# Optimization experiments

Measured on AMD Instinct MI355X. Metric: run time of the kernel, lower is better.

## Reference

```python
import jax, jax.numpy as jnp
import numpy as np

EPS = 1e-6


def setup_inputs() -> dict:
    key = jax.random.key(0)
    kH, kE1, kE2, kM, kW = jax.random.split(key, 5)
    B, N, D, E, L = 16, 2048, 64, 32768, 2
    H = jax.random.normal(kH, (B, N, D), dtype=jnp.float32)
    src = jax.random.randint(kE1, (B, 1, E), 0, N)
    dst = jax.random.randint(kE2, (B, 1, E), 0, N)
    edge_index = jnp.concatenate([src, dst], axis=1)  # [B, 2, E]
    m = jax.random.uniform(kM, (B, E), dtype=jnp.float32)
    W = jax.random.normal(kW, (L, D, D), dtype=jnp.float32) * (1.0 / np.sqrt(D))
    return {"H": H, "edge_index": edge_index, "m": m, "W": W}


def reference(H, edge_index, m, W):
    # H: [B, N, D]; edge_index: [B, 2, E] int; m: [B, E]; W: [L, D, D]
    B, N, _ = H.shape
    L = W.shape[0]
    bidx = jnp.arange(B)[:, None]          # [B, 1] broadcasts against [B, E]
    src = edge_index[:, 0, :]
    dst = edge_index[:, 1, :]
    A = jnp.zeros((B, N, N), dtype=H.dtype)
    # batched scatter: A[b, src, dst] = m; A[b, dst, src] = m (symmetric fill)
    A = A.at[bidx, src, dst].set(m)
    A = A.at[bidx, dst, src].set(m)
    A = A + jnp.eye(N, dtype=H.dtype)[None]  # add self loops
    deg = jnp.clip(A.sum(axis=-1), EPS)       # [B, N]
    dis = deg ** -0.5
    A_norm = dis[:, :, None] * A * dis[:, None, :]  # D^-1/2 A D^-1/2
    X = H
    for l in range(L):
        X = jnp.einsum('bnm,bmd->bnd', A_norm, X)
        X = jnp.einsum('bnd,ed->bne', X, W[l])  # Linear: X @ W^T
        if l < L - 1:
            X = jax.nn.gelu(X, approximate=False)  # torch GELU (exact erf); dropout in eval mode
    return X
```

## Files before the change

### kernel.cpp

```cpp
#include <hip/hip_runtime.h>
#include <stdint.h>
#include <math.h>

#define BATCH 16
#define NNODE 2048
#define DDIM  64
#define NEDGE 32768
#define SEG   32
#define SLOTS 128
#define NROWS (BATCH*NNODE)
#define RPB   128

__global__ void k_build(const int* __restrict__ ei, const float* __restrict__ m,
                        uint32_t* __restrict__ cnt4, uint2* __restrict__ entries) {
    __shared__ uint32_t cntS[RPB];
    __shared__ uint32_t keyS[RPB][SEG];
    __shared__ float    valS[RPB][SEG];

    int b  = blockIdx.x & 15;
    int gh = blockIdx.x >> 4;
    int r0 = (gh >> 2) * RPB;
    int q  = gh & 3;
    int t  = threadIdx.x;

    if (t < RPB) cntS[t] = 0u;
    __syncthreads();

    const int*   eb = ei + (size_t)b * 2 * NEDGE;
    const float* mb = m  + (size_t)b * NEDGE;
    int e0 = q * (NEDGE / 4);

    for (int i = 0; i < 4; ++i) {
        int e4 = e0 + i * 2048 + t * 4;
        int4   s4 = *(const int4*)(eb + e4);
        int4   d4 = *(const int4*)(eb + NEDGE + e4);
        float4 m4 = *(const float4*)(mb + e4);
        #pragma unroll
        for (int j = 0; j < 4; ++j) {
            int   src = j == 0 ? s4.x : j == 1 ? s4.y : j == 2 ? s4.z : s4.w;
            int   dst = j == 0 ? d4.x : j == 1 ? d4.y : j == 2 ? d4.z : d4.w;
            float mv  = j == 0 ? m4.x : j == 1 ? m4.y : j == 2 ? m4.z : m4.w;
            int e  = e4 + j;
            int rs = src - r0;
            if ((unsigned)rs < RPB) {
                uint32_t p = atomicAdd(&cntS[rs], 1u);
                if (p < SEG) { keyS[rs][p] = (uint32_t)dst | ((uint32_t)e << 11); valS[rs][p] = mv; }
            }
            int rd = dst - r0;
            if ((unsigned)rd < RPB) {
                uint32_t p = atomicAdd(&cntS[rd], 1u);
                if (p < SEG) { keyS[rd][p] = (uint32_t)src | ((uint32_t)(NEDGE + e) << 11); valS[rd][p] = mv; }
            }
        }
    }
    __syncthreads();

    int lane = t & 63;
    int wid  = t >> 6;
    int pos  = lane & 31;
    int sub  = lane >> 5;
    for (int rr = 0; rr < 8; ++rr) {
        int r  = wid * 16 + rr * 2 + sub;
        int rg = b * NNODE + r0 + r;
        int k  = (int)min(cntS[r], (uint32_t)SEG);
        size_t base = (size_t)rg * SLOTS + q * SEG;
        if (pos < k)
            entries[base + pos] = make_uint2(keyS[r][pos], __float_as_uint(valS[r][pos]));
        if (pos == 0) cnt4[rg * 4 + q] = (uint32_t)k;
    }
}

__global__ void k_dedupe(const uint32_t* __restrict__ cnt4, uint2* __restrict__ entries,
                         uint32_t* __restrict__ cnt_fin,
                         float* __restrict__ dis, float* __restrict__ self) {
    int b    = blockIdx.x & 15;
    int w    = b * NNODE + (blockIdx.x >> 4) * 4 + (threadIdx.x >> 6);
    int lane = threadIdx.x & 63;
    uint4 kq = ((const uint4*)cnt4)[w];
    int k0 = (int)kq.x, k1 = (int)kq.y, k2 = (int)kq.z, k3 = (int)kq.w;
    size_t base = (size_t)w * SLOTS;
    int pos = lane & 31;
    int klo = (lane < 32) ? k0 : k1;
    int khi = (lane < 32) ? k2 : k3;

    uint32_t key0 = 0u, key1 = 0u;
    float v0 = 0.f, v1 = 0.f;
    bool a0 = pos < klo;
    bool a1 = pos < khi;
    if (a0) { uint2 kv = entries[base + lane];      key0 = kv.x; v0 = __uint_as_float(kv.y); }
    if (a1) { uint2 kv = entries[base + 64 + lane]; key1 = kv.x; v1 = __uint_as_float(kv.y); }
    uint32_t c0 = key0 & 2047u, p0 = key0 >> 11;
    uint32_t c1 = key1 & 2047u, p1 = key1 >> 11;

    #define KILL(ks) { uint32_t cs = (ks) & 2047u, ps = (ks) >> 11; \
        a0 = a0 && !((c0 == cs) && (p0 < ps)); \
        a1 = a1 && !((c1 == cs) && (p1 < ps)); }
    for (int s = 0; s < k0; ++s) KILL(__builtin_amdgcn_readlane(key0, s))
    for (int s = 0; s < k1; ++s) KILL(__builtin_amdgcn_readlane(key0, 32 + s))
    for (int s = 0; s < k2; ++s) KILL(__builtin_amdgcn_readlane(key1, s))
    for (int s = 0; s < k3; ++s) KILL(__builtin_amdgcn_readlane(key1, 32 + s))
    #undef KILL

    float sum = (a0 ? v0 : 0.f) + (a1 ? v1 : 0.f);
    for (int off = 32; off; off >>= 1) sum += __shfl_xor(sum, off, 64);
    float deg = fmaxf(1.0f + sum, 1e-6f);
    if (lane == 0) {
        float di = 1.0f / sqrtf(deg);
        dis[w]  = di;
        self[w] = di * di;
    }

    unsigned long long m0 = __ballot(a0);
    unsigned long long m1 = __ballot(a1);
    unsigned long long below = (1ull << lane) - 1ull;
    int n0 = __popcll(m0);
    if (a0) entries[base + __popcll(m0 & below)]      = make_uint2(key0, __float_as_uint(v0));
    if (a1) entries[base + n0 + __popcll(m1 & below)] = make_uint2(key1, __float_as_uint(v1));
    if (lane == 0) cnt_fin[w] = (uint32_t)(n0 + __popcll(m1));
}

__global__ void k_layer(const float* __restrict__ Xin, const float* __restrict__ W,
                        float* __restrict__ Xout,
                        const uint32_t* __restrict__ cnt_fin, const uint2* __restrict__ entries,
                        const float* __restrict__ dis, const float* __restrict__ self,
                        int dogelu) {
    __shared__ float WT[64 * 65];
    int Lb = blockIdx.x;
    int b  = Lb & 15;
    int rb = Lb >> 4;
    int t  = threadIdx.x;

    #pragma unroll
    for (int i = 0; i < 16; ++i) {
        int idx = i * 256 + t;
        WT[(idx & 63) * 65 + (idx >> 6)] = W[idx];
    }
    __syncthreads();

    int lane = t & 63;
    int wid  = t >> 6;
    const float* Xb   = Xin + (size_t)b * NNODE * DDIM;
    const char*  Xc   = (const char*)Xb + lane * 4;
    const float* disB = dis + (b << 11);

    float accv[2];
    #pragma unroll
    for (int rr = 0; rr < 2; ++rr) {
        int row = rb * 8 + wid * 2 + rr;
        int rg  = b * NNODE + row;
        int k   = (int)cnt_fin[rg];
        size_t base = (size_t)rg * SLOTS;

        uint32_t kA = 0u, vA = 0u, kB = 0u, vB = 0u;
        if (lane < k)      { uint2 kv = entries[base + lane];      kA = kv.x; vA = kv.y; }
        if (lane + 64 < k) { uint2 kv = entries[base + 64 + lane]; kB = kv.x; vB = kv.y; }

        float dr = disB[row];
        int   colA = (int)(kA & 2047u);
        uint32_t offA = (uint32_t)colA << 8;
        uint32_t wAu  = __float_as_uint(__uint_as_float(vA) * dr * disB[colA]);
        int   colB = (int)(kB & 2047u);
        uint32_t offB = (uint32_t)colB << 8;
        uint32_t wBu  = __float_as_uint(__uint_as_float(vB) * dr * disB[colB]);

        float acc0 = self[rg] * Xb[(size_t)row * DDIM + lane];
        float acc1 = 0.f, acc2 = 0.f, acc3 = 0.f;

        int k0 = k < 64 ? k : 64;
        int e = 0;
        for (; e + 16 <= k0; e += 16) {
            float xv0, xv1, xv2, xv3, xv4, xv5, xv6, xv7;
            float xv8, xv9, xva, xvb, xvc, xvd, xve, xvf;
            float w0, w1, w2, w3, w4, w5, w6, w7;
            float w8, w9, wa, wb, wc, wd, we, wf;
            #define G(idx, X, Wv) { \
                uint32_t o = __builtin_amdgcn_readlane(offA, e + idx); \
                Wv = __uint_as_float(__builtin_amdgcn_readlane(wAu, e + idx)); \
                X = *(const float*)(Xc + o); }
            G(0, xv0, w0)  G(1, xv1, w1)  G(2, xv2, w2)  G(3, xv3, w3)
            G(4, xv4, w4)  G(5, xv5, w5)  G(6, xv6, w6)  G(7, xv7, w7)
            G(8, xv8, w8)  G(9, xv9, w9)  G(10, xva, wa) G(11, xvb, wb)
            G(12, xvc, wc) G(13, xvd, wd) G(14, xve, we) G(15, xvf, wf)
            #undef G
            acc0 = fmaf(w0, xv0, acc0); acc1 = fmaf(w1, xv1, acc1);
            acc2 = fmaf(w2, xv2, acc2); acc3 = fmaf(w3, xv3, acc3);
            acc0 = fmaf(w4, xv4, acc0); acc1 = fmaf(w5, xv5, acc1);
            acc2 = fmaf(w6, xv6, acc2); acc3 = fmaf(w7, xv7, acc3);
            acc0 = fmaf(w8, xv8, acc0); acc1 = fmaf(w9, xv9, acc1);
            acc2 = fmaf(wa, xva, acc2); acc3 = fmaf(wb, xvb, acc3);
            acc0 = fmaf(wc, xvc, acc0); acc1 = fmaf(wd, xvd, acc1);
            acc2 = fmaf(we, xve, acc2); acc3 = fmaf(wf, xvf, acc3);
        }
        for (; e + 4 <= k0; e += 4) {
            uint32_t o0 = __builtin_amdgcn_readlane(offA, e);
            uint32_t o1 = __builtin_amdgcn_readlane(offA, e + 1);
            uint32_t o2 = __builtin_amdgcn_readlane(offA, e + 2);
            uint32_t o3 = __builtin_amdgcn_readlane(offA, e + 3);
            float w0 = __uint_as_float(__builtin_amdgcn_readlane(wAu, e));
            float w1 = __uint_as_float(__builtin_amdgcn_readlane(wAu, e + 1));
            float w2 = __uint_as_float(__builtin_amdgcn_readlane(wAu, e + 2));
            float w3 = __uint_as_float(__builtin_amdgcn_readlane(wAu, e + 3));
            acc0 = fmaf(w0, *(const float*)(Xc + o0), acc0);
            acc1 = fmaf(w1, *(const float*)(Xc + o1), acc1);
            acc2 = fmaf(w2, *(const float*)(Xc + o2), acc2);
            acc3 = fmaf(w3, *(const float*)(Xc + o3), acc3);
        }
        for (; e < k0; ++e) {
            uint32_t o = __builtin_amdgcn_readlane(offA, e);
            float wv = __uint_as_float(__builtin_amdgcn_readlane(wAu, e));
            acc0 = fmaf(wv, *(const float*)(Xc + o), acc0);
        }
        for (e = 64; e < k; ++e) {
            uint32_t o = __builtin_amdgcn_readlane(offB, e - 64);
            float wv = __uint_as_float(__builtin_amdgcn_readlane(wBu, e - 64));
            acc1 = fmaf(wv, *(const float*)(Xc + o), acc1);
        }
        accv[rr] = (acc0 + acc1) + (acc2 + acc3);
    }

    float sa = accv[0], sb = accv[1];
    float ya = 0.f, yb = 0.f;
    #pragma unroll
    for (int d = 0; d < 64; ++d) {
        float wt = WT[d * 65 + lane];
        ya = fmaf(__uint_as_float(__builtin_amdgcn_readlane(__float_as_uint(sa), d)), wt, ya);
        yb = fmaf(__uint_as_float(__builtin_amdgcn_readlane(__float_as_uint(sb), d)), wt, yb);
    }
    if (dogelu) {
        ya = 0.5f * ya * (1.0f + erff(ya * 0.70710678118654752440f));
        yb = 0.5f * yb * (1.0f + erff(yb * 0.70710678118654752440f));
    }
    int row0 = rb * 8 + wid * 2;
    Xout[((size_t)b * NNODE + row0)     * DDIM + lane] = ya;
    Xout[((size_t)b * NNODE + row0 + 1) * DDIM + lane] = yb;
}

extern "C" void kernel_launch(void* const* d_in, const int* in_sizes, int n_in,
                              void* d_out, int out_size, void* d_ws, size_t ws_size,
                              hipStream_t stream) {
    const float* H  = (const float*)d_in[0];
    const int*   ei = (const int*)d_in[1];
    const float* m  = (const float*)d_in[2];
    const float* W  = (const float*)d_in[3];
    float* out = (float*)d_out;

    char* ws = (char*)d_ws;
    uint32_t* cnt4    = (uint32_t*)ws;
    uint32_t* cnt_fin = (uint32_t*)(ws + (512 << 10));
    float*    dis     = (float*)(ws + (640 << 10));
    float*    self    = (float*)(ws + (768 << 10));
    uint2*    entries = (uint2*)(ws + (896 << 10));
    float*    X2      = (float*)(ws + (896 << 10) + (size_t)NROWS * SLOTS * 8);

    k_build <<<BATCH * (NNODE / RPB) * 4, 512, 0, stream>>>(ei, m, cnt4, entries);
    k_dedupe<<<NROWS / 4, 256, 0, stream>>>(cnt4, entries, cnt_fin, dis, self);
    k_layer <<<4096, 256, 0, stream>>>(H,  W,        X2,  cnt_fin, entries, dis, self, 1);
    k_layer <<<4096, 256, 0, stream>>>(X2, W + 4096, out, cnt_fin, entries, dis, self, 0);
}
```

Before: 168.8 us.

## Process four rows per wavefront with interleaved gathers in layer kernel

Each wavefront of the layer kernel now handles four output rows instead of two. The row loops are interleaved so that gathered X loads from all four rows are issued together before any FMAs, which raises memory-level parallelism, and the grid is halved to match. This also amortizes the per-block W transpose into shared memory over twice as many rows. The cost is more registers, lower occupancy, and divergence-driven loops bounded by the longest row in the group.

Result: slower. 173.8 us (+3.0%).

```diff
diff --git a/kernel.cpp b/kernel.cpp
--- a/kernel.cpp
+++ b/kernel.cpp
@@ -143,96 +143,100 @@
     const char*  Xc   = (const char*)Xb + lane * 4;
     const float* disB = dis + (b << 11);
 
-    float accv[2];
-    #pragma unroll
-    for (int rr = 0; rr < 2; ++rr) {
-        int row = rb * 8 + wid * 2 + rr;
-        int rg  = b * NNODE + row;
-        int k   = (int)cnt_fin[rg];
+    int row0 = rb * 16 + wid * 4;
+    int rg0  = b * NNODE + row0;
+
+    uint32_t offA[4], wAu[4];
+    float acc0[4], acc1[4];
+    int kk[4], kc[4];
+    int kmax = 0;
+    #pragma unroll
+    for (int r = 0; r < 4; ++r) {
+        int rg = rg0 + r;
+        int k  = (int)cnt_fin[rg];
+        kk[r] = k;
         size_t base = (size_t)rg * SLOTS;
-
-        uint32_t kA = 0u, vA = 0u, kB = 0u, vB = 0u;
-        if (lane < k)      { uint2 kv = entries[base + lane];      kA = kv.x; vA = kv.y; }
-        if (lane + 64 < k) { uint2 kv = entries[base + 64 + lane]; kB = kv.x; vB = kv.y; }
-
-        float dr = disB[row];
-        int   colA = (int)(kA & 2047u);
-        uint32_t offA = (uint32_t)colA << 8;
-        uint32_t wAu  = __float_as_uint(__uint_as_float(vA) * dr * disB[colA]);
-        int   colB = (int)(kB & 2047u);
-        uint32_t offB = (uint32_t)colB << 8;
-        uint32_t wBu  = __float_as_uint(__uint_as_float(vB) * dr * disB[colB]);
-
-        float acc0 = self[rg] * Xb[(size_t)row * DDIM + lane];
-        float acc1 = 0.f, acc2 = 0.f, acc3 = 0.f;
-
-        int k0 = k < 64 ? k : 64;
-        int e = 0;
-        for (; e + 16 <= k0; e += 16) {
-            float xv0, xv1, xv2, xv3, xv4, xv5, xv6, xv7;
-            float xv8, xv9, xva, xvb, xvc, xvd, xve, xvf;
-            float w0, w1, w2, w3, w4, w5, w6, w7;
-            float w8, w9, wa, wb, wc, wd, we, wf;
-            #define G(idx, X, Wv) { \
-                uint32_t o = __builtin_amdgcn_readlane(offA, e + idx); \
-                Wv = __uint_as_float(__builtin_amdgcn_readlane(wAu, e + idx)); \
-                X = *(const float*)(Xc + o); }
-            G(0, xv0, w0)  G(1, xv1, w1)  G(2, xv2, w2)  G(3, xv3, w3)
-            G(4, xv4, w4)  G(5, xv5, w5)  G(6, xv6, w6)  G(7, xv7, w7)
-            G(8, xv8, w8)  G(9, xv9, w9)  G(10, xva, wa) G(11, xvb, wb)
-            G(12, xvc, wc) G(13, xvd, wd) G(14, xve, we) G(15, xvf, wf)
-            #undef G
-            acc0 = fmaf(w0, xv0, acc0); acc1 = fmaf(w1, xv1, acc1);
-            acc2 = fmaf(w2, xv2, acc2); acc3 = fmaf(w3, xv3, acc3);
-            acc0 = fmaf(w4, xv4, acc0); acc1 = fmaf(w5, xv5, acc1);
-            acc2 = fmaf(w6, xv6, acc2); acc3 = fmaf(w7, xv7, acc3);
-            acc0 = fmaf(w8, xv8, acc0); acc1 = fmaf(w9, xv9, acc1);
-            acc2 = fmaf(wa, xva, acc2); acc3 = fmaf(wb, xvb, acc3);
-            acc0 = fmaf(wc, xvc, acc0); acc1 = fmaf(wd, xvd, acc1);
-            acc2 = fmaf(we, xve, acc2); acc3 = fmaf(wf, xvf, acc3);
-        }
-        for (; e + 4 <= k0; e += 4) {
-            uint32_t o0 = __builtin_amdgcn_readlane(offA, e);
-            uint32_t o1 = __builtin_amdgcn_readlane(offA, e + 1);
-            uint32_t o2 = __builtin_amdgcn_readlane(offA, e + 2);
-            uint32_t o3 = __builtin_amdgcn_readlane(offA, e + 3);
-            float w0 = __uint_as_float(__builtin_amdgcn_readlane(wAu, e));
-            float w1 = __uint_as_float(__builtin_amdgcn_readlane(wAu, e + 1));
-            float w2 = __uint_as_float(__builtin_amdgcn_readlane(wAu, e + 2));
-            float w3 = __uint_as_float(__builtin_amdgcn_readlane(wAu, e + 3));
-            acc0 = fmaf(w0, *(const float*)(Xc + o0), acc0);
-            acc1 = fmaf(w1, *(const float*)(Xc + o1), acc1);
-            acc2 = fmaf(w2, *(const float*)(Xc + o2), acc2);
-            acc3 = fmaf(w3, *(const float*)(Xc + o3), acc3);
-        }
-        for (; e < k0; ++e) {
-            uint32_t o = __builtin_amdgcn_readlane(offA, e);
-            float wv = __uint_as_float(__builtin_amdgcn_readlane(wAu, e));
-            acc0 = fmaf(wv, *(const float*)(Xc + o), acc0);
-        }
-        for (e = 64; e < k; ++e) {
-            uint32_t o = __builtin_amdgcn_readlane(offB, e - 64);
-            float wv = __uint_as_float(__builtin_amdgcn_readlane(wBu, e - 64));
-            acc1 = fmaf(wv, *(const float*)(Xc + o), acc1);
-        }
-        accv[rr] = (acc0 + acc1) + (acc2 + acc3);
-    }
-
-    float sa = accv[0], sb = accv[1];
-    float ya = 0.f, yb = 0.f;
+        uint32_t kA = 0u, vA = 0u;
+        if (lane < k) { uint2 kv = entries[base + lane]; kA = kv.x; vA = kv.y; }
+        float dr  = disB[row0 + r];
+        int   col = (int)(kA & 2047u);
+        offA[r] = (uint32_t)col << 8;
+        wAu[r]  = __float_as_uint(__uint_as_float(vA) * dr * disB[col]);
+        acc0[r] = self[rg] * Xb[(size_t)(row0 + r) * DDIM + lane];
+        acc1[r] = 0.f;
+        int c = k < 64 ? k : 64;
+        kc[r] = c;
+        kmax = c > kmax ? c : kmax;
+    }
+
+    for (int e = 0; e < kmax; e += 4) {
+        float xv[4][4], wv[4][4];
+        #pragma unroll
+        for (int r = 0; r < 4; ++r) {
+            if (e < kc[r]) {
+                #pragma unroll
+                for (int j = 0; j < 4; ++j) {
+                    uint32_t o = __builtin_amdgcn_readlane(offA[r], e + j);
+                    wv[r][j] = __uint_as_float(__builtin_amdgcn_readlane(wAu[r], e + j));
+                    xv[r][j] = *(const float*)(Xc + o);
+                }
+            }
+        }
+        #pragma unroll
+        for (int r = 0; r < 4; ++r) {
+            if (e < kc[r]) {
+                acc0[r] = fmaf(wv[r][0], xv[r][0], acc0[r]);
+                acc1[r] = fmaf(wv[r][1], xv[r][1], acc1[r]);
+                acc0[r] = fmaf(wv[r][2], xv[r][2], acc0[r]);
+                acc1[r] = fmaf(wv[r][3], xv[r][3], acc1[r]);
+            }
+        }
+    }
+
+    #pragma unroll
+    for (int r = 0; r < 4; ++r) {
+        int k = kk[r];
+        if (k > 64) {
+            int rg = rg0 + r;
+            size_t base = (size_t)rg * SLOTS;
+            uint32_t kB = 0u, vB = 0u;
+            if (lane + 64 < k) { uint2 kv = entries[base + 64 + lane]; kB = kv.x; vB = kv.y; }
+            float dr  = disB[row0 + r];
+            int   col = (int)(kB & 2047u);
+            uint32_t offB = (uint32_t)col << 8;
+            uint32_t wBu  = __float_as_uint(__uint_as_float(vB) * dr * disB[col]);
+            for (int e2 = 64; e2 < k; ++e2) {
+                uint32_t o  = __builtin_amdgcn_readlane(offB, e2 - 64);
+                float    wvv = __uint_as_float(__builtin_amdgcn_readlane(wBu, e2 - 64));
+                acc1[r] = fmaf(wvv, *(const float*)(Xc + o), acc1[r]);
+            }
+        }
+    }
+
+    float s0 = acc0[0] + acc1[0];
+    float s1 = acc0[1] + acc1[1];
+    float s2 = acc0[2] + acc1[2];
+    float s3 = acc0[3] + acc1[3];
+    float y0 = 0.f, y1 = 0.f, y2 = 0.f, y3 = 0.f;
     #pragma unroll
     for (int d = 0; d < 64; ++d) {
         float wt = WT[d * 65 + lane];
-        ya = fmaf(__uint_as_float(__builtin_amdgcn_readlane(__float_as_uint(sa), d)), wt, ya);
-        yb = fmaf(__uint_as_float(__builtin_amdgcn_readlane(__float_as_uint(sb), d)), wt, yb);
+        y0 = fmaf(__uint_as_float(__builtin_amdgcn_readlane(__float_as_uint(s0), d)), wt, y0);
+        y1 = fmaf(__uint_as_float(__builtin_amdgcn_readlane(__float_as_uint(s1), d)), wt, y1);
+        y2 = fmaf(__uint_as_float(__builtin_amdgcn_readlane(__float_as_uint(s2), d)), wt, y2);
+        y3 = fmaf(__uint_as_float(__builtin_amdgcn_readlane(__float_as_uint(s3), d)), wt, y3);
     }
     if (dogelu) {
-        ya = 0.5f * ya * (1.0f + erff(ya * 0.70710678118654752440f));
-        yb = 0.5f * yb * (1.0f + erff(yb * 0.70710678118654752440f));
-    }
-    int row0 = rb * 8 + wid * 2;
-    Xout[((size_t)b * NNODE + row0)     * DDIM + lane] = ya;
-    Xout[((size_t)b * NNODE + row0 + 1) * DDIM + lane] = yb;
+        y0 = 0.5f * y0 * (1.0f + erff(y0 * 0.70710678118654752440f));
+        y1 = 0.5f * y1 * (1.0f + erff(y1 * 0.70710678118654752440f));
+        y2 = 0.5f * y2 * (1.0f + erff(y2 * 0.70710678118654752440f));
+        y3 = 0.5f * y3 * (1.0f + erff(y3 * 0.70710678118654752440f));
+    }
+    size_t ob = ((size_t)b * NNODE + row0) * DDIM + lane;
+    Xout[ob]            = y0;
+    Xout[ob + DDIM]     = y1;
+    Xout[ob + 2 * DDIM] = y2;
+    Xout[ob + 3 * DDIM] = y3;
 }
 
 extern "C" void kernel_launch(void* const* d_in, const int* in_sizes, int n_in,
@@ -254,6 +258,6 @@
 
     k_build <<<BATCH * (NNODE / RPB) * 4, 512, 0, stream>>>(ei, m, cnt4, entries);
     k_dedupe<<<NROWS / 4, 256, 0, stream>>>(cnt4, entries, cnt_fin, dis, self);
-    k_layer <<<4096, 256, 0, stream>>>(H,  W,        X2,  cnt_fin, entries, dis, self, 1);
-    k_layer <<<4096, 256, 0, stream>>>(X2, W + 4096, out, cnt_fin, entries, dis, self, 0);
-}
+    k_layer <<<BATCH * (NNODE / 16), 256, 0, stream>>>(H,  W,        X2,  cnt_fin, entries, dis, self, 1);
+    k_layer <<<BATCH * (NNODE / 16), 256, 0, stream>>>(X2, W + 4096, out, cnt_fin, entries, dis, self, 0);
+}
```
